# Optimization experiments

Hardware: AMD Instinct MI355X
Metric: run time of the kernel (lower is better)

Reference implementation:

```python
import jax, jax.numpy as jnp
import numpy as np

N = 100_000   # nodes
E = 6_400_000 # edges
R = 90        # relations
NB = 3        # num_blocks


def setup_inputs() -> dict:
    key = jax.random.key(0)
    ks = jax.random.split(key, 10)
    x = jax.random.normal(ks[0], (N, 3), jnp.float32)
    edge_index = jax.random.randint(ks[1], (2, E), 0, N, dtype=jnp.int32)
    edge_type = jax.random.randint(ks[2], (E,), 0, R, dtype=jnp.int32)
    batch = jnp.zeros((N,), jnp.int32)  # single graph, as in source
    p = lambda k, shape: (jax.random.normal(k, shape, jnp.float32) * 0.1)
    # block-diagonal weights: [R, NB, in_b, out_b]
    W1, root1, b1 = p(ks[3], (R, NB, 1, 2)), p(ks[4], (3, 6)), jnp.zeros((6,), jnp.float32)
    W2, root2, b2 = p(ks[5], (R, NB, 2, 1)), p(ks[6], (6, 3)), jnp.zeros((3,), jnp.float32)
    W3, root3, b3 = p(ks[7], (R, NB, 1, 2)), p(ks[8], (3, 6)), jnp.zeros((6,), jnp.float32)
    return dict(x=x, edge_index=edge_index, batch=batch, edge_type=edge_type,
                W1=W1, root1=root1, b1=b1, W2=W2, root2=root2, b2=b2,
                W3=W3, root3=root3, b3=b3)


def _rgcn(x, src, dst, edge_type, W, root, bias, aggr):
    # block-diagonal per-relation transform of gathered source features
    nb, in_b, out_b = W.shape[1], W.shape[2], W.shape[3]
    xb = x[src].reshape(-1, nb, in_b)                      # [E, NB, in_b]
    msg = jnp.einsum('ebi,ebio->ebo', xb, W[edge_type])    # [E, NB, out_b]
    msg = msg.reshape(-1, nb * out_b)                      # [E, out]
    if aggr == 'mean':
        # per-(dst node, relation) normalization, as in FastRGCNConv
        comb = dst * R + edge_type                         # [E]
        cnt = jax.ops.segment_sum(jnp.ones((msg.shape[0],), msg.dtype), comb,
                                  num_segments=N * R)      # [N*R]
        msg = msg / jnp.clip(cnt[comb], 1.0)[:, None]
    agg = jax.ops.segment_sum(msg, dst, num_segments=N)    # [N, out]
    return agg + x @ root + bias


def reference(x, edge_index, batch, edge_type, W1, root1, b1, W2, root2, b2, W3, root3, b3):
    src, dst = edge_index[0], edge_index[1]
    h = jax.nn.relu(_rgcn(x, src, dst, edge_type, W1, root1, b1, 'mean'))
    # dropout is identity in eval mode
    h = jax.nn.relu(_rgcn(h, src, dst, edge_type, W2, root2, b2, 'add'))
    h = jax.nn.relu(_rgcn(h, src, dst, edge_type, W3, root3, b3, 'mean'))
    # global mean pool over batch (single graph here, kept general)
    num_graphs = 1
    s = jax.ops.segment_sum(h, batch, num_segments=num_graphs)
    c = jax.ops.segment_sum(jnp.ones((h.shape[0],), h.dtype), batch, num_segments=num_graphs)
    pooled = s / jnp.clip(c, 1.0)[:, None]
    return jax.nn.log_softmax(pooled, axis=1)
```

## Files before the change

### kernel.cpp

```cpp
#include <hip/hip_runtime.h>


#define NREL   90
#define BSH    7
#define BNODES 128
#define NBINS  1024
#define GCH    10240
#define CAPB   11264
#define NV4    6
#define STAGE  9088
#define LPD    16

__device__ __forceinline__ float frelu(float v) { return v > 0.0f ? v : 0.0f; }

__launch_bounds__(512)
__global__ void group_k(const float* __restrict__ x, float4* __restrict__ x4,
                        int N, int gNp,
                        const int* __restrict__ src, const int* __restrict__ dst,
                        const int* __restrict__ et, int* __restrict__ gcount,
                        unsigned* __restrict__ regions, int E) {
    int tid = threadIdx.x;
    if (blockIdx.x < gNp) {
        int i = blockIdx.x * 512 + tid;
        if (i < N) x4[i] = make_float4(x[3 * i], x[3 * i + 1], x[3 * i + 2], 0.0f);
        return;
    }
    __shared__ int s_hist[NBINS];
    __shared__ int s_cur[NBINS];
    __shared__ int s_off[NBINS];
    __shared__ unsigned s_pack[GCH];
    int chunk = blockIdx.x - gNp;
    int e0 = chunk * GCH;
    int cnt = min(GCH, E - e0);
    for (int i = tid; i < NBINS; i += 512) s_hist[i] = 0;
    __syncthreads();
#pragma unroll 4
    for (int q = tid; q < cnt; q += 512)
        atomicAdd(&s_hist[dst[e0 + q] >> BSH], 1);
    __syncthreads();
    if (tid < 64) {
        int loc[16];
        int s = 0;
        int b0 = tid * 16;
#pragma unroll
        for (int k = 0; k < 16; k++) { loc[k] = s_hist[b0 + k]; s += loc[k]; }
        int inc = s;
#pragma unroll
        for (int off = 1; off < 64; off <<= 1) {
            int u = __shfl_up(inc, off);
            if (tid >= off) inc += u;
        }
        int run = inc - s;
#pragma unroll
        for (int k = 0; k < 16; k++) { s_cur[b0 + k] = run; run += loc[k]; }
    }
    __syncthreads();
    for (int b = tid; b < NBINS; b += 512) {
        int len = s_hist[b];
        if (len > 0) {
            int padded = (len + 7) & ~7;
            int gb = atomicAdd(&gcount[b], padded);
            unsigned* reg = regions + (size_t)b * CAPB;
            if (gb + padded <= CAPB) {
                s_off[b] = gb - s_cur[b];
                for (int j = gb + len; j < gb + padded; j++) reg[j] = 0xFFFFFFFFu;
            } else {
                s_off[b] = 0x40000000;
                for (int j = gb; j < CAPB; j++) reg[j] = 0xFFFFFFFFu;
            }
        } else s_off[b] = 0x40000000;
    }
    __syncthreads();
#pragma unroll 4
    for (int q = tid; q < cnt; q += 512) {
        int e = e0 + q;
        int d = dst[e];
        int b = d >> BSH;
        int p = atomicAdd(&s_cur[b], 1);
        s_pack[p] = (unsigned)src[e] | ((unsigned)et[e] << 17) |
                    ((unsigned)(d & (BNODES - 1)) << 24);
    }
    __syncthreads();
#pragma unroll 2
    for (int i = tid; i < cnt; i += 512) {
        int lo = 0, hi = NBINS - 1;
        while (lo < hi) {
            int mid = (lo + hi) >> 1;
            if (s_cur[mid] > i) hi = mid; else lo = mid + 1;
        }
        int loc = s_off[lo] + i;
        if (loc < CAPB) regions[(size_t)lo * CAPB + loc] = s_pack[i];
    }
}

__launch_bounds__(512)
__global__ void sortb_l1_k(const int* __restrict__ gcount, unsigned* regions,
                           int2* __restrict__ rowseg,
                           const float4* __restrict__ x4, const float* __restrict__ W,
                           const float* __restrict__ root, const float* __restrict__ bias,
                           float4* __restrict__ h1p, int N) {
    __shared__ unsigned stage32[STAGE];
    __shared__ unsigned hist8w[BNODES * 90 / 4];
    __shared__ int hh[BNODES], cur[BNODES], base_[BNODES];
    __shared__ float4 w4[NREL * 2];
    int tid = threadIdx.x, b = blockIdx.x;
    for (int i = tid; i < BNODES * 90 / 4; i += 512) hist8w[i] = 0u;
    for (int i = tid; i < NREL * 2; i += 512) {
        int r = i >> 1;
        w4[i] = (i & 1) ? make_float4(W[r * 6 + 4], W[r * 6 + 5], 0.f, 0.f)
                        : make_float4(W[r * 6], W[r * 6 + 1], W[r * 6 + 2], W[r * 6 + 3]);
    }
    __syncthreads();
    int fill = gcount[b];
    if (fill > CAPB) fill = CAPB;
    const uint4* reg4 = (const uint4*)(regions + (size_t)b * CAPB);
    int nv = fill >> 2;
    uint4 rec4[NV4];
#define HIST1(P) if ((P) != 0xFFFFFFFFu) { \
        unsigned bi_ = ((P) >> 24) * 90u + (((P) >> 17) & 127u); \
        atomicAdd(&hist8w[bi_ >> 2], 1u << ((bi_ & 3) << 3)); }
#pragma unroll
    for (int k = 0; k < NV4; k++) {
        int i4 = tid + k * 512;
        if (i4 < nv) {
            uint4 v = reg4[i4];
            rec4[k] = v;
            HIST1(v.x); HIST1(v.y); HIST1(v.z); HIST1(v.w);
        } else {
            rec4[k] = make_uint4(0xFFFFFFFFu, 0xFFFFFFFFu, 0xFFFFFFFFu, 0xFFFFFFFFu);
        }
    }
    __syncthreads();
    if (tid < BNODES) {
        const unsigned char* h8 = (const unsigned char*)hist8w;
        unsigned s = 0;
        for (int k = 0; k < 90; k++) s += h8[tid * 90 + k];
        hh[tid] = (int)s;
    }
    __syncthreads();
    if (tid < 64) {
        int c0 = hh[2 * tid], c1 = hh[2 * tid + 1];
        int s = c0 + c1;
        int inc = s;
#pragma unroll
        for (int off = 1; off < 64; off <<= 1) {
            int u = __shfl_up(inc, off);
            if (tid >= off) inc += u;
        }
        int run = inc - s;
        base_[2 * tid] = run;          cur[2 * tid] = run;
        base_[2 * tid + 1] = run + c0; cur[2 * tid + 1] = run + c0;
    }
    __syncthreads();
    int cntv = base_[BNODES - 1] + hh[BNODES - 1];
    if (tid < BNODES) {
        int d = (b << BSH) + tid;
        if (d < N) {
            int beg = base_[tid];
            int end = beg + hh[tid];
            if (end > cntv) end = cntv;
            rowseg[d] = make_int2(b * CAPB + beg, b * CAPB + end);
        }
    }
#define PLACE1(P) if ((P) != 0xFFFFFFFFu) { \
        int pos_ = atomicAdd(&cur[(P) >> 24], 1); \
        if (pos_ < STAGE) stage32[pos_] = (P); }
#pragma unroll
    for (int k = 0; k < NV4; k++) {
        PLACE1(rec4[k].x); PLACE1(rec4[k].y); PLACE1(rec4[k].z); PLACE1(rec4[k].w);
    }
    __syncthreads();
    unsigned* regw = regions + (size_t)b * CAPB;
    int grp = tid >> 4, l16 = tid & 15;
#pragma unroll
    for (int rd = 0; rd < 4; rd++) {
        int dL = grp + rd * 32;
        int segb = base_[dL];
        int sege = segb + hh[dL];
        if (sege > cntv) sege = cntv;
        float a0 = 0, a1 = 0, a2 = 0, a3 = 0, a4 = 0, a5 = 0;
        for (int q = segb + l16; q < sege; q += 16) {
            unsigned p = stage32[q];
            unsigned rel = (p >> 17) & 127u;
            unsigned bi = dL * 90u + rel;
            unsigned c = (hist8w[bi >> 2] >> ((bi & 3) << 3)) & 0xFFu;
            regw[q] = (p & 0x00FFFFFFu) | (c << 24);
            float r = __builtin_amdgcn_rcpf((float)c);
            float4 xv = x4[p & 0x1FFFFu];
            unsigned rel2 = rel * 2u;
            float4 wa = w4[rel2], wb = w4[rel2 + 1];
            float x0 = xv.x * r, x1 = xv.y * r, x2 = xv.z * r;
            a0 += x0 * wa.x; a1 += x0 * wa.y;
            a2 += x1 * wa.z; a3 += x1 * wa.w;
            a4 += x2 * wb.x; a5 += x2 * wb.y;
        }
#pragma unroll
        for (int off = 8; off > 0; off >>= 1) {
            a0 += __shfl_down(a0, off); a1 += __shfl_down(a1, off); a2 += __shfl_down(a2, off);
            a3 += __shfl_down(a3, off); a4 += __shfl_down(a4, off); a5 += __shfl_down(a5, off);
        }
        if (l16 == 0) {
            int d = (b << BSH) + dL;
            if (d < N) {
                float4 xv = x4[d];
                float o[6] = {a0, a1, a2, a3, a4, a5};
#pragma unroll
                for (int j = 0; j < 6; j++)
                    o[j] = frelu(o[j] + xv.x * root[j] + xv.y * root[6 + j] +
                                 xv.z * root[12 + j] + bias[j]);
                h1p[d * 2]     = make_float4(o[0], o[1], o[2], o[3]);
                h1p[d * 2 + 1] = make_float4(o[4], o[5], 0.0f, 0.0f);
            }
        }
    }
}

__launch_bounds__(256)
__global__ void l2_g(const int2* __restrict__ rowseg, const unsigned* __restrict__ sorted,
                     const float4* __restrict__ h1p, const float* __restrict__ W,
                     const float* __restrict__ root, const float* __restrict__ bias,
                     float4* __restrict__ h2p, int N) {
    __shared__ float4 w4[NREL * 2];
    for (int i = threadIdx.x; i < NREL * 2; i += 256) {
        int r = i >> 1;
        w4[i] = (i & 1) ? make_float4(W[r * 6 + 4], W[r * 6 + 5], 0.f, 0.f)
                        : make_float4(W[r * 6], W[r * 6 + 1], W[r * 6 + 2], W[r * 6 + 3]);
    }
    __syncthreads();
    int grp = threadIdx.x >> 4, l16 = threadIdx.x & 15;
    int d = blockIdx.x * LPD + grp;
    if (d >= N) return;
    int2 sg = rowseg[d];
    int beg = sg.x, end = sg.y;
    float a0 = 0, a1 = 0, a2 = 0;
    int i = beg + l16;
    for (; i + 48 < end; i += 64) {
        unsigned p[4];
        float4 ha[4], hb[4];
#pragma unroll
        for (int k = 0; k < 4; k++) p[k] = sorted[i + k * 16];
#pragma unroll
        for (int k = 0; k < 4; k++) {
            unsigned s = p[k] & 0x1FFFFu;
            ha[k] = h1p[2 * s]; hb[k] = h1p[2 * s + 1];
        }
#pragma unroll
        for (int k = 0; k < 4; k++) {
            unsigned rel2 = ((p[k] >> 17) & 127u) * 2u;
            float4 wa = w4[rel2], wb = w4[rel2 + 1];
            a0 += ha[k].x * wa.x + ha[k].y * wa.y;
            a1 += ha[k].z * wa.z + ha[k].w * wa.w;
            a2 += hb[k].x * wb.x + hb[k].y * wb.y;
        }
    }
    for (; i < end; i += 16) {
        unsigned p = sorted[i];
        unsigned s = p & 0x1FFFFu;
        float4 ha = h1p[2 * s], hb = h1p[2 * s + 1];
        unsigned rel2 = ((p >> 17) & 127u) * 2u;
        float4 wa = w4[rel2], wb = w4[rel2 + 1];
        a0 += ha.x * wa.x + ha.y * wa.y;
        a1 += ha.z * wa.z + ha.w * wa.w;
        a2 += hb.x * wb.x + hb.y * wb.y;
    }
#pragma unroll
    for (int off = 8; off > 0; off >>= 1) {
        a0 += __shfl_down(a0, off); a1 += __shfl_down(a1, off); a2 += __shfl_down(a2, off);
    }
    if (l16 == 0) {
        float4 ha = h1p[2 * d], hb = h1p[2 * d + 1];
        float hv[6] = {ha.x, ha.y, ha.z, ha.w, hb.x, hb.y};
        float o[3] = {a0, a1, a2};
#pragma unroll
        for (int j = 0; j < 3; j++) {
            float v = o[j] + bias[j];
#pragma unroll
            for (int k = 0; k < 6; k++) v += hv[k] * root[k * 3 + j];
            o[j] = frelu(v);
        }
        h2p[d] = make_float4(o[0], o[1], o[2], 0.0f);
    }
}

__launch_bounds__(256)
__global__ void l3_g(const int2* __restrict__ rowseg, const unsigned* __restrict__ sorted,
                     const float4* __restrict__ h2p, const float* __restrict__ W,
                     const float* __restrict__ root, const float* __restrict__ bias,
                     const int* __restrict__ batch, float* __restrict__ partials, int N) {
    __shared__ float4 w4[NREL * 2];
    __shared__ float redsm[LPD][8];
    for (int i = threadIdx.x; i < NREL * 2; i += 256) {
        int r = i >> 1;
        w4[i] = (i & 1) ? make_float4(W[r * 6 + 4], W[r * 6 + 5], 0.f, 0.f)
                        : make_float4(W[r * 6], W[r * 6 + 1], W[r * 6 + 2], W[r * 6 + 3]);
    }
    __syncthreads();
    int grp = threadIdx.x >> 4, l16 = threadIdx.x & 15;
    int d = blockIdx.x * LPD + grp;
    float a0 = 0, a1 = 0, a2 = 0, a3 = 0, a4 = 0, a5 = 0;
    if (d < N) {
        int2 sg = rowseg[d];
        int beg = sg.x, end = sg.y;
        int i = beg + l16;
        for (; i + 48 < end; i += 64) {
            unsigned p[4];
            float4 xv[4];
#pragma unroll
            for (int k = 0; k < 4; k++) p[k] = sorted[i + k * 16];
#pragma unroll
            for (int k = 0; k < 4; k++) xv[k] = h2p[p[k] & 0x1FFFFu];
#pragma unroll
            for (int k = 0; k < 4; k++) {
                float r = __builtin_amdgcn_rcpf((float)(p[k] >> 24));
                unsigned rel2 = ((p[k] >> 17) & 127u) * 2u;
                float4 wa = w4[rel2], wb = w4[rel2 + 1];
                float x0 = xv[k].x * r, x1 = xv[k].y * r, x2 = xv[k].z * r;
                a0 += x0 * wa.x; a1 += x0 * wa.y;
                a2 += x1 * wa.z; a3 += x1 * wa.w;
                a4 += x2 * wb.x; a5 += x2 * wb.y;
            }
        }
        for (; i < end; i += 16) {
            unsigned p = sorted[i];
            float r = __builtin_amdgcn_rcpf((float)(p >> 24));
            float4 xv = h2p[p & 0x1FFFFu];
            unsigned rel2 = ((p >> 17) & 127u) * 2u;
            float4 wa = w4[rel2], wb = w4[rel2 + 1];
            float x0 = xv.x * r, x1 = xv.y * r, x2 = xv.z * r;
            a0 += x0 * wa.x; a1 += x0 * wa.y;
            a2 += x1 * wa.z; a3 += x1 * wa.w;
            a4 += x2 * wb.x; a5 += x2 * wb.y;
        }
    }
#pragma unroll
    for (int off = 8; off > 0; off >>= 1) {
        a0 += __shfl_down(a0, off); a1 += __shfl_down(a1, off); a2 += __shfl_down(a2, off);
        a3 += __shfl_down(a3, off); a4 += __shfl_down(a4, off); a5 += __shfl_down(a5, off);
    }
    if (l16 == 0) {
        float v[7] = {0, 0, 0, 0, 0, 0, 0};
        if (d < N && batch[d] == 0) {
            float4 xv = h2p[d];
            float o[6] = {a0, a1, a2, a3, a4, a5};
#pragma unroll
            for (int j = 0; j < 6; j++)
                v[j] = frelu(o[j] + xv.x * root[j] + xv.y * root[6 + j] +
                             xv.z * root[12 + j] + bias[j]);
            v[6] = 1.0f;
        }
#pragma unroll
        for (int k = 0; k < 7; k++) redsm[grp][k] = v[k];
    }
    __syncthreads();
    if (threadIdx.x < 7) {
        float t = 0;
#pragma unroll
        for (int g = 0; g < LPD; g++) t += redsm[g][threadIdx.x];
        partials[(size_t)blockIdx.x * 8 + threadIdx.x] = t;
    }
}

__global__ void pool_finalize(const float* __restrict__ partials, int nb,
                              float* __restrict__ out) {
    float v[7] = {0, 0, 0, 0, 0, 0, 0};
    for (int b = threadIdx.x; b < nb; b += blockDim.x) {
#pragma unroll
        for (int k = 0; k < 7; k++) v[k] += partials[(size_t)b * 8 + k];
    }
#pragma unroll
    for (int off = 32; off > 0; off >>= 1) {
#pragma unroll
        for (int k = 0; k < 7; k++) v[k] += __shfl_down(v[k], off);
    }
    __shared__ float sm[16][8];
    int wv = threadIdx.x >> 6, lane = threadIdx.x & 63;
    if (lane == 0) {
#pragma unroll
        for (int k = 0; k < 7; k++) sm[wv][k] = v[k];
    }
    __syncthreads();
    if (threadIdx.x == 0) {
        float t[7] = {0, 0, 0, 0, 0, 0, 0};
        int nw = blockDim.x >> 6;
        for (int q = 0; q < nw; q++) {
#pragma unroll
            for (int k = 0; k < 7; k++) t[k] += sm[q][k];
        }
        float c = t[6] < 1.0f ? 1.0f : t[6];
        float p[6], m = -1e30f;
#pragma unroll
        for (int j = 0; j < 6; j++) { p[j] = t[j] / c; m = fmaxf(m, p[j]); }
        float s = 0.0f;
#pragma unroll
        for (int j = 0; j < 6; j++) s += expf(p[j] - m);
        float lse = m + logf(s);
#pragma unroll
        for (int j = 0; j < 6; j++) out[j] = p[j] - lse;
    }
}

extern "C" void kernel_launch(void* const* d_in, const int* in_sizes, int n_in,
                              void* d_out, int out_size, void* d_ws, size_t ws_size,
                              hipStream_t stream) {
    const float* x     = (const float*)d_in[0];
    const int*   ei    = (const int*)d_in[1];
    const int*   batch = (const int*)d_in[2];
    const int*   etype = (const int*)d_in[3];
    const float* W1    = (const float*)d_in[4];
    const float* root1 = (const float*)d_in[5];
    const float* b1    = (const float*)d_in[6];
    const float* W2    = (const float*)d_in[7];
    const float* root2 = (const float*)d_in[8];
    const float* b2    = (const float*)d_in[9];
    const float* W3    = (const float*)d_in[10];
    const float* root3 = (const float*)d_in[11];
    const float* b3    = (const float*)d_in[12];

    const int N = in_sizes[0] / 3;
    const int E = in_sizes[1] / 2;
    const int* src = ei;
    const int* dst = ei + E;
    const int gG = (E + GCH - 1) / GCH;
    const int NBUCK = (N + BNODES - 1) >> BSH;
    const int gL = (N + LPD - 1) / LPD;

    char* ws = (char*)d_ws;
    size_t off = 0;
    auto alloc = [&](size_t bytes) -> void* {
        void* p = ws + off;
        off += (bytes + 255) & ~(size_t)255;
        return p;
    };
    int*      gcount  = (int*)     alloc(NBINS * sizeof(int));
    size_t zero_bytes = off;
    unsigned* regions = (unsigned*)alloc((size_t)NBUCK * CAPB * sizeof(unsigned));
    int2*     rowseg  = (int2*)    alloc((size_t)N * sizeof(int2));
    float4*   x4      = (float4*)  alloc((size_t)N * sizeof(float4));
    float4*   h1p     = (float4*)  alloc((size_t)N * 2 * sizeof(float4));
    float4*   h2p     = (float4*)  alloc((size_t)N * sizeof(float4));
    float*    partials = (float*)  alloc((size_t)gL * 8 * sizeof(float));

    hipMemsetAsync(d_ws, 0, zero_bytes, stream);

    const int gNp = (N + 511) / 512;

    group_k<<<gNp + gG, 512, 0, stream>>>(x, x4, N, gNp, src, dst, etype,
                                          gcount, regions, E);
    sortb_l1_k<<<NBUCK, 512, 0, stream>>>(gcount, regions, rowseg,
                                          x4, W1, root1, b1, h1p, N);
    l2_g<<<gL, 256, 0, stream>>>(rowseg, regions, h1p, W2, root2, b2, h2p, N);
    l3_g<<<gL, 256, 0, stream>>>(rowseg, regions, h2p, W3, root3, b3, batch, partials, N);
    pool_finalize<<<1, 1024, 0, stream>>>(partials, gL, (float*)d_out);
}
```

Before: 323.3 us.

## Single-pass edge bucketing with register-held records and vectorized region writes

The grouping kernel now reads each edge's dst/src/type once into registers, building both the histogram and the packed records in that one pass, where before it read dst twice. Bins are padded to multiples of 4 inside shared memory and pre-filled with sentinels, so the scatter to global regions can be done with uint4 stores instead of scalar stores. Chunk size and region capacity are reduced and the bin count is trimmed to the 784 buckets actually needed. The trade-offs are higher register pressure from 17 records per thread and smaller regions that could overflow for skewed inputs.

```diff
diff --git a/kernel.cpp b/kernel.cpp
--- a/kernel.cpp
+++ b/kernel.cpp
@@ -5,11 +5,15 @@
 #define BSH    7
 #define BNODES 128
 #define NBINS  1024
-#define GCH    10240
-#define CAPB   11264
+#define NB2    784
+#define GCH    8704
+#define KPT    17
+#define SPK    11056
+#define CAPB   10496
 #define NV4    6
 #define STAGE  9088
 #define LPD    16
+#define SENT   0xFFFFFFFFu
 
 __device__ __forceinline__ float frelu(float v) { return v > 0.0f ? v : 0.0f; }
 
@@ -25,25 +29,39 @@
         if (i < N) x4[i] = make_float4(x[3 * i], x[3 * i + 1], x[3 * i + 2], 0.0f);
         return;
     }
-    __shared__ int s_hist[NBINS];
-    __shared__ int s_cur[NBINS];
-    __shared__ int s_off[NBINS];
-    __shared__ unsigned s_pack[GCH];
+    __shared__ int s_cur[NB2];
+    __shared__ int s_pend[NB2];
+    __shared__ int s_off[NB2];
+    __shared__ unsigned s_pack[SPK];
     int chunk = blockIdx.x - gNp;
     int e0 = chunk * GCH;
     int cnt = min(GCH, E - e0);
-    for (int i = tid; i < NBINS; i += 512) s_hist[i] = 0;
-    __syncthreads();
-#pragma unroll 4
-    for (int q = tid; q < cnt; q += 512)
-        atomicAdd(&s_hist[dst[e0 + q] >> BSH], 1);
-    __syncthreads();
-    if (tid < 64) {
+    for (int i = tid; i < NB2; i += 512) s_pend[i] = 0;
+    __syncthreads();
+    unsigned rec[KPT];
+    int bkt[KPT];
+#pragma unroll
+    for (int k = 0; k < KPT; k++) {
+        int q = tid + k * 512;
+        if (q < cnt) {
+            int e = e0 + q;
+            int d = dst[e];
+            bkt[k] = d >> BSH;
+            rec[k] = (unsigned)src[e] | ((unsigned)et[e] << 17) |
+                     ((unsigned)(d & (BNODES - 1)) << 24);
+            atomicAdd(&s_pend[bkt[k]], 1);
+        } else bkt[k] = -1;
+    }
+    __syncthreads();
+    if (tid < 49) {
         int loc[16];
         int s = 0;
         int b0 = tid * 16;
 #pragma unroll
-        for (int k = 0; k < 16; k++) { loc[k] = s_hist[b0 + k]; s += loc[k]; }
+        for (int k = 0; k < 16; k++) {
+            int plen = (s_pend[b0 + k] + 3) & ~3;
+            loc[k] = plen; s += plen;
+        }
         int inc = s;
 #pragma unroll
         for (int off = 1; off < 64; off <<= 1) {
@@ -52,44 +70,52 @@
         }
         int run = inc - s;
 #pragma unroll
-        for (int k = 0; k < 16; k++) { s_cur[b0 + k] = run; run += loc[k]; }
-    }
-    __syncthreads();
-    for (int b = tid; b < NBINS; b += 512) {
-        int len = s_hist[b];
-        if (len > 0) {
-            int padded = (len + 7) & ~7;
-            int gb = atomicAdd(&gcount[b], padded);
-            unsigned* reg = regions + (size_t)b * CAPB;
-            if (gb + padded <= CAPB) {
-                s_off[b] = gb - s_cur[b];
-                for (int j = gb + len; j < gb + padded; j++) reg[j] = 0xFFFFFFFFu;
+        for (int k = 0; k < 16; k++) {
+            s_cur[b0 + k] = run;
+            run += loc[k];
+            s_pend[b0 + k] = run;
+        }
+    }
+    __syncthreads();
+    int T = s_pend[NB2 - 1];
+    for (int b = tid; b < NB2; b += 512) {
+        int st = s_cur[b];
+        int plen = s_pend[b] - st;
+        if (plen > 0) {
+            int gb = atomicAdd(&gcount[b], plen);
+            if (gb + plen <= CAPB) {
+                s_off[b] = gb - st;
             } else {
                 s_off[b] = 0x40000000;
-                for (int j = gb; j < CAPB; j++) reg[j] = 0xFFFFFFFFu;
+                unsigned* reg = regions + (size_t)b * CAPB;
+                for (int j = min(gb, CAPB); j < CAPB; j++) reg[j] = SENT;
             }
         } else s_off[b] = 0x40000000;
     }
-    __syncthreads();
-#pragma unroll 4
-    for (int q = tid; q < cnt; q += 512) {
-        int e = e0 + q;
-        int d = dst[e];
-        int b = d >> BSH;
-        int p = atomicAdd(&s_cur[b], 1);
-        s_pack[p] = (unsigned)src[e] | ((unsigned)et[e] << 17) |
-                    ((unsigned)(d & (BNODES - 1)) << 24);
-    }
-    __syncthreads();
-#pragma unroll 2
-    for (int i = tid; i < cnt; i += 512) {
-        int lo = 0, hi = NBINS - 1;
+    for (int i = tid; i < T; i += 512) s_pack[i] = SENT;
+    __syncthreads();
+#pragma unroll
+    for (int k = 0; k < KPT; k++) {
+        if (bkt[k] >= 0) {
+            int p = atomicAdd(&s_cur[bkt[k]], 1);
+            s_pack[p] = rec[k];
+        }
+    }
+    __syncthreads();
+    int nv = T >> 2;
+    for (int i4 = tid; i4 < nv; i4 += 512) {
+        int i = i4 << 2;
+        int lo = 0, hi = NB2 - 1;
         while (lo < hi) {
             int mid = (lo + hi) >> 1;
-            if (s_cur[mid] > i) hi = mid; else lo = mid + 1;
+            if (s_pend[mid] > i) hi = mid; else lo = mid + 1;
         }
         int loc = s_off[lo] + i;
-        if (loc < CAPB) regions[(size_t)lo * CAPB + loc] = s_pack[i];
+        if (loc < CAPB) {
+            uint4 v = make_uint4(s_pack[i], s_pack[i + 1],
+                                 s_pack[i + 2], s_pack[i + 3]);
+            *(uint4*)(regions + (size_t)lo * CAPB + loc) = v;
+        }
     }
 }
 
@@ -116,7 +142,7 @@
     const uint4* reg4 = (const uint4*)(regions + (size_t)b * CAPB);
     int nv = fill >> 2;
     uint4 rec4[NV4];
-#define HIST1(P) if ((P) != 0xFFFFFFFFu) { \
+#define HIST1(P) if ((P) != SENT) { \
         unsigned bi_ = ((P) >> 24) * 90u + (((P) >> 17) & 127u); \
         atomicAdd(&hist8w[bi_ >> 2], 1u << ((bi_ & 3) << 3)); }
 #pragma unroll
@@ -127,7 +153,7 @@
             rec4[k] = v;
             HIST1(v.x); HIST1(v.y); HIST1(v.z); HIST1(v.w);
         } else {
-            rec4[k] = make_uint4(0xFFFFFFFFu, 0xFFFFFFFFu, 0xFFFFFFFFu, 0xFFFFFFFFu);
+            rec4[k] = make_uint4(SENT, SENT, SENT, SENT);
         }
     }
     __syncthreads();
@@ -162,7 +188,7 @@
             rowseg[d] = make_int2(b * CAPB + beg, b * CAPB + end);
         }
     }
-#define PLACE1(P) if ((P) != 0xFFFFFFFFu) { \
+#define PLACE1(P) if ((P) != SENT) { \
         int pos_ = atomicAdd(&cur[(P) >> 24], 1); \
         if (pos_ < STAGE) stage32[pos_] = (P); }
 #pragma unroll
```

Result: faster. 291.2 us (-9.9%).
